# Kernel tuning notes

Measured on AMD Instinct MI355X. Metric: run time of the kernel, lower is better.

Reference implementation:

```python
import jax, jax.numpy as jnp
import numpy as np

B, S, H, W, DF, D, HID, ITERS = 8, 8, 64, 64, 64, 64, 128, 3
EPS = 1e-8


def build_grid(h, w):
    ranges = [np.linspace(-1.0, 1.0, num=h), np.linspace(-1.0, 1.0, num=w)]
    g = np.meshgrid(*ranges, sparse=False, indexing='xy')
    return jnp.asarray(np.stack(g, axis=-1), dtype=jnp.float32)  # [H, W, 2]


def ln(x, g, b):
    m = jnp.mean(x, axis=-1, keepdims=True)
    v = jnp.mean((x - m) ** 2, axis=-1, keepdims=True)
    return (x - m) * jax.lax.rsqrt(v + 1e-5) * g + b


def setup_inputs() -> dict:
    key = jax.random.key(0)
    ks = iter(jax.random.split(key, 64))
    def nrm(shape, s=0.02):
        return jax.random.normal(next(ks), shape, jnp.float32) * s
    inp = {}
    inp['inputs'] = jax.random.normal(next(ks), (B, H, W, DF), jnp.float32)
    # learned slot inits and learned per-slot position / scale factors
    inp['slots_p'] = jax.random.normal(next(ks), (1, S, D), jnp.float32)
    inp['s_pos_p'] = 2.0 * jax.random.uniform(next(ks), (1, S, 2), jnp.float32) - 1.0
    inp['s_scale_p'] = 0.1 + 0.01 * jax.random.normal(next(ks), (1, S, 2), jnp.float32)
    # soft position embedding Linear(2, D)
    inp['W_pos'] = nrm((2, D)); inp['b_pos'] = jnp.zeros((D,), jnp.float32)
    # q/k/v projections
    inp['Wq'] = nrm((D, D)); inp['bq'] = jnp.zeros((D,), jnp.float32)
    inp['Wk'] = nrm((DF, D)); inp['bk'] = jnp.zeros((D,), jnp.float32)
    inp['Wv'] = nrm((DF, D)); inp['bv'] = jnp.zeros((D,), jnp.float32)
    # layernorms
    inp['g_in'] = jnp.ones((DF,), jnp.float32); inp['b_in'] = jnp.zeros((DF,), jnp.float32)
    inp['g_slots'] = jnp.ones((D,), jnp.float32); inp['b_slots'] = jnp.zeros((D,), jnp.float32)
    inp['g_k'] = jnp.ones((D,), jnp.float32); inp['b_k'] = jnp.zeros((D,), jnp.float32)
    inp['g_v'] = jnp.ones((D,), jnp.float32); inp['b_v'] = jnp.zeros((D,), jnp.float32)
    # shared kv MLP fc1_kv / fc2_kv
    inp['W1'] = nrm((D, 2 * D)); inp['b1'] = jnp.zeros((2 * D,), jnp.float32)
    inp['W2'] = nrm((2 * D, D)); inp['b2'] = jnp.zeros((D,), jnp.float32)
    # GRUCell (torch layout transposed to [in, 3*D])
    inp['W_ih'] = nrm((D, 3 * D)); inp['b_ih'] = jnp.zeros((3 * D,), jnp.float32)
    inp['W_hh'] = nrm((D, 3 * D)); inp['b_hh'] = jnp.zeros((3 * D,), jnp.float32)
    # residual slot MLP
    inp['g_pre'] = jnp.ones((D,), jnp.float32); inp['b_pre'] = jnp.zeros((D,), jnp.float32)
    inp['Wf1'] = nrm((D, HID)); inp['bf1'] = jnp.zeros((HID,), jnp.float32)
    inp['Wf2'] = nrm((HID, D)); inp['bf2'] = jnp.zeros((D,), jnp.float32)
    return inp


def reference(inputs, slots_p, s_pos_p, s_scale_p, W_pos, b_pos, Wq, bq, Wk, bk, Wv, bv,
              g_in, b_in, g_slots, b_slots, g_k, b_k, g_v, b_v, W1, b1, W2, b2,
              W_ih, W_hh, b_ih, b_hh, g_pre, b_pre, Wf1, bf1, Wf2, bf2):
    grid = build_grid(H, W)                 # [H, W, 2]
    grid_flat = grid.reshape(-1, 2)          # [HW, 2]
    scale = D ** (-0.5)

    x = ln(inputs, g_in, b_in)
    k0 = x @ Wk + bk                         # [B, H, W, D]
    v0 = x @ Wv + bv

    slots = jnp.broadcast_to(slots_p, (B, S, D))
    s_pos = jnp.clip(jnp.broadcast_to(s_pos_p, (B, S, 2)), -1.0, 1.0)[:, :, None, None, :]
    s_scale = jnp.clip(jnp.broadcast_to(s_scale_p, (B, S, 2)), 1e-3, 2.0)[:, :, None, None, :]

    def proj_kv(base, sp, ss, g, b):
        gr = (grid[None, None] - sp) / (ss * 5.0)      # [B, S, H, W, 2]
        pe = gr @ W_pos + b_pos                        # [B, S, H, W, D]
        t = (base[:, None] + pe).reshape(B, S, H * W, D)
        t = ln(t, g, b)
        return jax.nn.relu(t @ W1 + b1) @ W2 + b2      # [B, S, HW, D]

    for i in range(ITERS + 1):
        slots_prev = slots
        q = ln(slots, g_slots, b_slots) @ Wq + bq       # [B, S, D]
        kk = proj_kv(k0, s_pos, s_scale, g_k, b_k)
        vv = proj_kv(v0, s_pos, s_scale, g_v, b_v)
        dots = jnp.einsum('bid,bijd->bij', q, kk) * scale
        attn_mask = jax.nn.softmax(dots, axis=1) + EPS  # softmax over slot axis
        attn = attn_mask / jnp.sum(attn_mask, axis=-1, keepdims=True)
        updates = jnp.einsum('bijd,bij->bid', vv, attn)
        if i < ITERS:
            xg = updates.reshape(-1, D) @ W_ih + b_ih
            hg = slots_prev.reshape(-1, D) @ W_hh + b_hh
            ir, iz, inn = jnp.split(xg, 3, axis=-1)
            hr, hz, hn = jnp.split(hg, 3, axis=-1)
            r = jax.nn.sigmoid(ir + hr)
            z = jax.nn.sigmoid(iz + hz)
            n = jnp.tanh(inn + r * hn)
            slots = ((1.0 - z) * n + z * slots_prev.reshape(-1, D)).reshape(B, S, D)
            slots = slots + (jax.nn.relu(ln(slots, g_pre, b_pre) @ Wf1 + bf1) @ Wf2 + bf2)
        else:
            slots = slots_prev
        # update per-slot position / scale from the attention mask
        sp = jnp.einsum('bij,jd->bid', attn_mask, grid_flat) / jnp.sum(attn_mask, axis=-1, keepdims=True)
        diff = grid_flat[None, None] - sp[:, :, None]   # [B, S, HW, 2]
        am = attn_mask + 1e-8
        ss = jnp.sqrt(jnp.einsum('bij,bijd->bid', am, diff ** 2) / jnp.sum(am, axis=-1, keepdims=True))
        s_pos = sp[:, :, None, None, :]
        s_scale = jnp.clip(ss, 1e-3, 2.0)[:, :, None, None, :]
    return slots, s_pos, s_scale, attn_mask
```

## Files before the change

kernel.cpp:

```cpp
#include <hip/hip_runtime.h>
#include <math.h>

typedef __bf16 bf16_t;
typedef __bf16 bfrag __attribute__((ext_vector_type(8)));
typedef float ffrag __attribute__((ext_vector_type(4)));

__device__ __forceinline__ float wave_sum(float v) {
#pragma unroll
  for (int m = 32; m >= 1; m >>= 1) v += __shfl_xor(v, m, 64);
  return v;
}
__device__ __forceinline__ float lin_(int i) { return -1.f + (2.f * (float)i) / 63.f; }
__device__ __forceinline__ float bflo(unsigned u) { return __uint_as_float(u << 16); }
__device__ __forceinline__ float bfhi(unsigned u) { return __uint_as_float(u & 0xFFFF0000u); }

__global__ __launch_bounds__(256) void k_setup(
    const float* __restrict__ slots_p, const float* __restrict__ s_pos_p,
    const float* __restrict__ s_scale_p, const float* __restrict__ W1,
    const float* __restrict__ b1, const float* __restrict__ g_k,
    const float* __restrict__ b_k, const float* __restrict__ g_v,
    const float* __restrict__ b_v, const float* __restrict__ W_pos,
    const float* __restrict__ b_pos, const float* __restrict__ Wk,
    const float* __restrict__ Wv,
    float* __restrict__ slotsS, float* __restrict__ sposS,
    float* __restrict__ sscaleS, float* __restrict__ momentsHsum,
    bf16_t* __restrict__ W1kT, bf16_t* __restrict__ W1vT,
    bf16_t* __restrict__ WkT, bf16_t* __restrict__ WvT,
    float4* __restrict__ nckA, float* __restrict__ nckB,
    float4* __restrict__ ncvA, float* __restrict__ ncvB,
    float* __restrict__ possum) {
  int t = threadIdx.x;
  for (int i = t; i < 8512; i += 256) momentsHsum[i] = 0.f;
  for (int i = t; i < 4096; i += 256) slotsS[i] = slots_p[i & 511];
  if (t < 128) {
    sposS[t] = fminf(fmaxf(s_pos_p[t & 15], -1.f), 1.f);
    sscaleS[t] = fminf(fmaxf(s_scale_p[t & 15], 0.001f), 2.f);
  }
  for (int i = t; i < 4096; i += 256) {
    int n = i >> 6, d = i & 63;
    WkT[i] = (bf16_t)Wk[d * 64 + n];
    WvT[i] = (bf16_t)Wv[d * 64 + n];
  }
  if (t < 128) {
    int n = t;
    float wxk = 0, wyk = 0, wbk = 0, uk = 0, sk = 0;
    float wxv = 0, wyv = 0, wbv = 0, uv = 0, sv = 0;
    for (int c = 0; c < 64; ++c) {
      float w = W1[c * 128 + n];
      float wk = g_k[c] * w, wv = g_v[c] * w;
      W1kT[n * 64 + c] = (bf16_t)wk;
      W1vT[n * 64 + c] = (bf16_t)wv;
      float px = W_pos[c], py = W_pos[64 + c], bp = b_pos[c];
      wxk += px * wk; wyk += py * wk; wbk += bp * wk; sk += wk; uk += b_k[c] * w;
      wxv += px * wv; wyv += py * wv; wbv += bp * wv; sv += wv; uv += b_v[c] * w;
    }
    nckA[n] = make_float4(wxk, wyk, wbk, uk + b1[n]); nckB[n] = sk;
    ncvA[n] = make_float4(wxv, wyv, wbv, uv + b1[n]); ncvB[n] = sv;
  }
  if (t < 64) {
    float px = W_pos[t], py = W_pos[64 + t], bp = b_pos[t];
    float s[9] = {px, py, bp, px * px, py * py, bp * bp, px * py, px * bp, py * bp};
#pragma unroll
    for (int i = 0; i < 9; ++i) {
      float v = wave_sum(s[i]);
      if (t == 0) possum[i] = v;
    }
  }
}

__device__ __forceinline__ void pass_type(
    const bf16_t xs[][72], bf16_t t0s[][72],
    const bf16_t WTl[][72], const bf16_t W1l[][72],
    const float* __restrict__ bias, const float* wpxs, const float* wpys,
    const float* bpvs, float* __restrict__ statsG, bf16_t* __restrict__ P0G,
    int j0, int wv, int lq, int ln15) {
  ffrag C[4] = {{0,0,0,0},{0,0,0,0},{0,0,0,0},{0,0,0,0}};
#pragma unroll
  for (int ks = 0; ks < 2; ++ks) {
    bfrag a = *(const bfrag*)&xs[wv * 16 + ln15][ks * 32 + lq * 8];
#pragma unroll
    for (int nt = 0; nt < 4; ++nt) {
      bfrag bb = *(const bfrag*)&WTl[nt * 16 + ln15][ks * 32 + lq * 8];
      C[nt] = __builtin_amdgcn_mfma_f32_16x16x32_bf16(a, bb, C[nt], 0, 0, 0);
    }
  }
  float kv[4][4];
  float st[5][4];
#pragma unroll
  for (int i = 0; i < 5; ++i)
#pragma unroll
    for (int rg = 0; rg < 4; ++rg) st[i][rg] = 0.f;
#pragma unroll
  for (int nt = 0; nt < 4; ++nt) {
    int n = nt * 16 + ln15;
    float bn = bias[n], pxw = wpxs[n], pyw = wpys[n], bpw = bpvs[n];
#pragma unroll
    for (int rg = 0; rg < 4; ++rg) {
      float v = C[nt][rg] + bn;
      kv[nt][rg] = v;
      st[0][rg] += v; st[1][rg] += v * v; st[2][rg] += v * pxw;
      st[3][rg] += v * pyw; st[4][rg] += v * bpw;
    }
  }
#pragma unroll
  for (int i = 0; i < 5; ++i)
#pragma unroll
    for (int rg = 0; rg < 4; ++rg) {
      float v = st[i][rg];
      v += __shfl_xor(v, 1, 64); v += __shfl_xor(v, 2, 64);
      v += __shfl_xor(v, 4, 64); v += __shfl_xor(v, 8, 64);
      st[i][rg] = v;
    }
  if (ln15 == 0) {
#pragma unroll
    for (int rg = 0; rg < 4; ++rg) {
      int j = j0 + wv * 16 + lq * 4 + rg;
#pragma unroll
      for (int i = 0; i < 5; ++i) statsG[j * 5 + i] = st[i][rg];
    }
  }
#pragma unroll
  for (int nt = 0; nt < 4; ++nt)
#pragma unroll
    for (int rg = 0; rg < 4; ++rg)
      t0s[wv * 16 + lq * 4 + rg][nt * 16 + ln15] = (bf16_t)kv[nt][rg];
  ffrag D[8] = {{0,0,0,0},{0,0,0,0},{0,0,0,0},{0,0,0,0},
                {0,0,0,0},{0,0,0,0},{0,0,0,0},{0,0,0,0}};
#pragma unroll
  for (int ks = 0; ks < 2; ++ks) {
    bfrag a = *(const bfrag*)&t0s[wv * 16 + ln15][ks * 32 + lq * 8];
#pragma unroll
    for (int nt = 0; nt < 8; ++nt) {
      bfrag bb = *(const bfrag*)&W1l[nt * 16 + ln15][ks * 32 + lq * 8];
      D[nt] = __builtin_amdgcn_mfma_f32_16x16x32_bf16(a, bb, D[nt], 0, 0, 0);
    }
  }
#pragma unroll
  for (int nt = 0; nt < 8; ++nt)
#pragma unroll
    for (int rg = 0; rg < 4; ++rg)
      P0G[(size_t)(j0 + wv * 16 + lq * 4 + rg) * 128 + nt * 16 + ln15] =
          (bf16_t)D[nt][rg];
}

__global__ __launch_bounds__(256) void k_pre(
    const float* __restrict__ inp, const float* __restrict__ g_in,
    const float* __restrict__ b_in, const float* __restrict__ bk,
    const float* __restrict__ bv, const bf16_t* __restrict__ WkT,
    const bf16_t* __restrict__ WvT, const bf16_t* __restrict__ W1kT,
    const bf16_t* __restrict__ W1vT, const float* __restrict__ W_pos,
    const float* __restrict__ b_pos,
    bf16_t* __restrict__ P0k, bf16_t* __restrict__ P0v,
    float* __restrict__ statsK, float* __restrict__ statsV,
    const float* __restrict__ slotsS, const float* __restrict__ g_slots,
    const float* __restrict__ b_slots, const float* __restrict__ Wq,
    const float* __restrict__ bq, const float* __restrict__ W2,
    const float* __restrict__ b2, float* __restrict__ w2qg,
    float* __restrict__ b2qg) {
  __shared__ bf16_t xs[64][72];
  __shared__ bf16_t t0s[64][72];
  __shared__ bf16_t WkTl[64][72];
  __shared__ bf16_t WvTl[64][72];
  __shared__ bf16_t W1kl[128][72];
  __shared__ bf16_t W1vl[128][72];
  __shared__ float wpxs[64], wpys[64], bpvs[64];
  const int tid = threadIdx.x;
  const int j0 = blockIdx.x * 64;
  for (int i = tid; i < 512; i += 256) {
    int row = i >> 3, seg = i & 7;
    *(uint4*)&WkTl[row][seg * 8] = ((const uint4*)WkT)[i];
    *(uint4*)&WvTl[row][seg * 8] = ((const uint4*)WvT)[i];
  }
  for (int i = tid; i < 1024; i += 256) {
    int row = i >> 3, seg = i & 7;
    *(uint4*)&W1kl[row][seg * 8] = ((const uint4*)W1kT)[i];
    *(uint4*)&W1vl[row][seg * 8] = ((const uint4*)W1vT)[i];
  }
  if (tid < 64) { wpxs[tid] = W_pos[tid]; wpys[tid] = W_pos[64 + tid]; bpvs[tid] = b_pos[tid]; }
  {
    const int px = tid >> 2, cg = tid & 3;
    const float* rowp = inp + (size_t)(j0 + px) * 64 + cg * 16;
    float v[16];
    *(float4*)&v[0]  = ((const float4*)rowp)[0];
    *(float4*)&v[4]  = ((const float4*)rowp)[1];
    *(float4*)&v[8]  = ((const float4*)rowp)[2];
    *(float4*)&v[12] = ((const float4*)rowp)[3];
    float s = 0.f, s2 = 0.f;
#pragma unroll
    for (int i = 0; i < 16; ++i) { s += v[i]; s2 += v[i] * v[i]; }
    s += __shfl_xor(s, 1, 64); s += __shfl_xor(s, 2, 64);
    s2 += __shfl_xor(s2, 1, 64); s2 += __shfl_xor(s2, 2, 64);
    float m = s * 0.015625f;
    float r = rsqrtf(s2 * 0.015625f - m * m + 1e-5f);
    float g[16], bb[16];
    *(float4*)&g[0]  = ((const float4*)(g_in + cg * 16))[0];
    *(float4*)&g[4]  = ((const float4*)(g_in + cg * 16))[1];
    *(float4*)&g[8]  = ((const float4*)(g_in + cg * 16))[2];
    *(float4*)&g[12] = ((const float4*)(g_in + cg * 16))[3];
    *(float4*)&bb[0]  = ((const float4*)(b_in + cg * 16))[0];
    *(float4*)&bb[4]  = ((const float4*)(b_in + cg * 16))[1];
    *(float4*)&bb[8]  = ((const float4*)(b_in + cg * 16))[2];
    *(float4*)&bb[12] = ((const float4*)(b_in + cg * 16))[3];
#pragma unroll
    for (int e = 0; e < 8; ++e) {
      float x0 = (v[2 * e] - m) * r * g[2 * e] + bb[2 * e];
      float x1 = (v[2 * e + 1] - m) * r * g[2 * e + 1] + bb[2 * e + 1];
      union { unsigned u; bf16_t h[2]; } cv;
      cv.h[0] = (bf16_t)x0; cv.h[1] = (bf16_t)x1;
      *(unsigned*)&xs[px][cg * 16 + 2 * e] = cv.u;
    }
  }
  __syncthreads();
  const int wv = tid >> 6, lane = tid & 63, lq = lane >> 4, ln15 = lane & 15;
  pass_type(xs, t0s, WkTl, W1kl, bk, wpxs, wpys, bpvs, statsK, P0k, j0, wv, lq, ln15);
  pass_type(xs, t0s, WvTl, W1vl, bv, wpxs, wpys, bpvs, statsV, P0v, j0, wv, lq, ln15);
  if (blockIdx.x < 64 && tid < 64) {
    int bs = blockIdx.x, d = tid;
    float v = slotsS[bs * 64 + d];
    float m = wave_sum(v) * 0.015625f;
    float c = v - m;
    float var = wave_sum(c * c) * 0.015625f;
    float xn = c * rsqrtf(var + 1e-5f) * g_slots[d] + b_slots[d];
    float q = bq[d];
    for (int cc = 0; cc < 64; ++cc) q = fmaf(__shfl(xn, cc, 64), Wq[cc * 64 + d], q);
    float w0 = 0.f, w1 = 0.f;
    for (int cc = 0; cc < 64; ++cc) {
      float qc = __shfl(q, cc, 64);
      w0 = fmaf(W2[d * 64 + cc], qc, w0);
      w1 = fmaf(W2[(64 + d) * 64 + cc], qc, w1);
    }
    w2qg[bs * 128 + d] = w0;
    w2qg[bs * 128 + 64 + d] = w1;
    float p = wave_sum(b2[d] * q);
    if (d == 0) b2qg[bs] = p;
  }
}

template <int LAST>
__global__ __launch_bounds__(256) void k_iter(
    const bf16_t* __restrict__ P0kg, const bf16_t* __restrict__ P0vg,
    const float* __restrict__ statsK, const float* __restrict__ statsV,
    const float4* __restrict__ nckA, const float* __restrict__ nckB,
    const float4* __restrict__ ncvA, const float* __restrict__ ncvB,
    const float* __restrict__ possum, const float* __restrict__ w2qg,
    const float* __restrict__ b2qg, const float* __restrict__ sposS,
    const float* __restrict__ sscaleS, float* __restrict__ moments,
    float* __restrict__ Hsum, float* __restrict__ outAttn) {
  __shared__ unsigned P0kl[64 * 65];
  __shared__ unsigned P0vl[64 * 65];
  __shared__ float4 nckAl[128];
  __shared__ float nckBl[128];
  __shared__ float w2qTl[128][8];
  __shared__ float4 scalV[64][9];
  __shared__ float attnS[64][10];
  __shared__ float HsumW[4][8][128];
  __shared__ float momAcc[8][5];
  const int tid = threadIdx.x;
  const int tile = blockIdx.x, b = blockIdx.y;
  const int jg0 = b * 4096 + tile * 64;
#pragma unroll
  for (int r = 0; r < 4; ++r) {
    int idx = tid + 256 * r;
    int row = idx >> 4, seg = idx & 15;
    uint4 v = ((const uint4*)P0kg)[(size_t)(jg0 + row) * 16 + seg];
    unsigned* dst = &P0kl[row * 65 + seg * 4];
    dst[0] = v.x; dst[1] = v.y; dst[2] = v.z; dst[3] = v.w;
    if (!LAST) {
      uint4 w = ((const uint4*)P0vg)[(size_t)(jg0 + row) * 16 + seg];
      unsigned* d2 = &P0vl[row * 65 + seg * 4];
      d2[0] = w.x; d2[1] = w.y; d2[2] = w.z; d2[3] = w.w;
    }
  }
  if (tid < 128) { nckAl[tid] = nckA[tid]; nckBl[tid] = nckB[tid]; }
#pragma unroll
  for (int r = 0; r < 4; ++r) {
    int idx = tid + 256 * r;
    int s = idx >> 7, n = idx & 127;
    w2qTl[n][s] = w2qg[(b * 8 + s) * 128 + n];
  }
  if (tid < 40) momAcc[tid / 5][tid % 5] = 0.f;
  float4 ncv0 = {0, 0, 0, 0}, ncv1 = {0, 0, 0, 0};
  float wsv0 = 0.f, wsv1 = 0.f;
  if (!LAST) {
    int l = tid & 63;
    ncv0 = ncvA[l]; ncv1 = ncvA[l + 64];
    wsv0 = ncvB[l]; wsv1 = ncvB[l + 64];
  }
  __syncthreads();

  const int px = tid >> 2, sp = tid & 3;
  const int jimg = tile * 64 + px;
  const float gx = lin_(jimg & 63), gy = lin_(jimg >> 6);
  const float Swx = possum[0], Swy = possum[1], Sbp = possum[2];
  const float Swx2 = possum[3], Swy2 = possum[4], Sbp2 = possum[5];
  const float Swxy = possum[6], Swxb = possum[7], Swyb = possum[8];
  float skA[5], svA[5];
#pragma unroll
  for (int i = 0; i < 5; ++i) {
    skA[i] = statsK[(size_t)(jg0 + px) * 5 + i];
    svA[i] = statsV[(size_t)(jg0 + px) * 5 + i];
  }
  float c1a[8], c2a[8], rKa[8], mrKa[8];
#pragma unroll
  for (int s = 0; s < 8; ++s) {
    int bs = b * 8 + s;
    float spx = sposS[bs * 2], spy = sposS[bs * 2 + 1];
    float rxx = 1.f / (sscaleS[bs * 2] * 5.f);
    float ryy = 1.f / (sscaleS[bs * 2 + 1] * 5.f);
    float c1 = (gx - spx) * rxx, c2 = (gy - spy) * ryy;
    float quad = c1 * c1 * Swx2 + c2 * c2 * Swy2 + Sbp2 +
                 2.f * (c1 * c2 * Swxy + c1 * Swxb + c2 * Swyb);
    float mK = (skA[0] + c1 * Swx + c2 * Swy + Sbp) * 0.015625f;
    float e2K = (skA[1] + 2.f * (c1 * skA[2] + c2 * skA[3] + skA[4]) + quad) * 0.015625f;
    float rK = rsqrtf(e2K - mK * mK + 1e-5f);
    c1a[s] = c1; c2a[s] = c2; rKa[s] = rK; mrKa[s] = mK * rK;
    if (!LAST && (s >> 1) == sp) {
      float mV = (svA[0] + c1 * Swx + c2 * Swy + Sbp) * 0.015625f;
      float e2V = (svA[1] + 2.f * (c1 * svA[2] + c2 * svA[3] + svA[4]) + quad) * 0.015625f;
      float rV = rsqrtf(e2V - mV * mV + 1e-5f);
      scalV[px][s] = make_float4(c1, c2, rV, mV * rV);
    }
  }
  float d8[8] = {0, 0, 0, 0, 0, 0, 0, 0};
#pragma unroll 4
  for (int i = 0; i < 16; ++i) {
    int k = sp * 16 + i;
    unsigned u = P0kl[px * 65 + k];
    float p0 = bflo(u), p1 = bfhi(u);
    float4 A0 = nckAl[2 * k], A1 = nckAl[2 * k + 1];
    float ws0 = nckBl[2 * k], ws1 = nckBl[2 * k + 1];
    float4 q0a = *(const float4*)&w2qTl[2 * k][0];
    float4 q0b = *(const float4*)&w2qTl[2 * k][4];
    float4 q1a = *(const float4*)&w2qTl[2 * k + 1][0];
    float4 q1b = *(const float4*)&w2qTl[2 * k + 1][4];
    float qq0[8] = {q0a.x, q0a.y, q0a.z, q0a.w, q0b.x, q0b.y, q0b.z, q0b.w};
    float qq1[8] = {q1a.x, q1a.y, q1a.z, q1a.w, q1b.x, q1b.y, q1b.z, q1b.w};
    float bm0 = p0 + A0.z, bm1 = p1 + A1.z;
#pragma unroll
    for (int s = 0; s < 8; ++s) {
      float z0 = bm0 + c1a[s] * A0.x + c2a[s] * A0.y;
      float h0 = fmaxf(fmaf(rKa[s], z0, fmaf(-mrKa[s], ws0, A0.w)), 0.f);
      d8[s] = fmaf(h0, qq0[s], d8[s]);
      float z1 = bm1 + c1a[s] * A1.x + c2a[s] * A1.y;
      float h1 = fmaxf(fmaf(rKa[s], z1, fmaf(-mrKa[s], ws1, A1.w)), 0.f);
      d8[s] = fmaf(h1, qq1[s], d8[s]);
    }
  }
#pragma unroll
  for (int s = 0; s < 8; ++s) {
    float v = d8[s];
    v += __shfl_xor(v, 1, 64);
    v += __shfl_xor(v, 2, 64);
    d8[s] = (v + b2qg[b * 8 + s]) * 0.125f;
  }
  float mx = d8[0];
#pragma unroll
  for (int s = 1; s < 8; ++s) mx = fmaxf(mx, d8[s]);
  float tt = 0.f;
  float e8[8];
#pragma unroll
  for (int s = 0; s < 8; ++s) { e8[s] = expf(d8[s] - mx); tt += e8[s]; }
  float inv = 1.f / tt;
#pragma unroll
  for (int s = 0; s < 8; ++s) e8[s] = e8[s] * inv + 1e-8f;
  float wa, wb;
  if (sp == 0) { wa = e8[0]; wb = e8[1]; }
  else if (sp == 1) { wa = e8[2]; wb = e8[3]; }
  else if (sp == 2) { wa = e8[4]; wb = e8[5]; }
  else { wa = e8[6]; wb = e8[7]; }
  *(float2*)&attnS[px][sp * 2] = make_float2(wa, wb);
  if (LAST) {
    outAttn[(size_t)(b * 8 + sp * 2) * 4096 + jimg] = wa;
    outAttn[(size_t)(b * 8 + sp * 2 + 1) * 4096 + jimg] = wb;
  }
  {
    float mm[10] = {wa, wa * gx, wa * gy, wa * gx * gx, wa * gy * gy,
                    wb, wb * gx, wb * gy, wb * gx * gx, wb * gy * gy};
#pragma unroll
    for (int i = 0; i < 10; ++i) {
      float v = mm[i];
      v += __shfl_xor(v, 4, 64); v += __shfl_xor(v, 8, 64);
      v += __shfl_xor(v, 16, 64); v += __shfl_xor(v, 32, 64);
      mm[i] = v;
    }
    if ((tid & 63) < 4) {
#pragma unroll
      for (int i = 0; i < 5; ++i) {
        atomicAdd(&momAcc[sp * 2][i], mm[i]);
        atomicAdd(&momAcc[sp * 2 + 1][i], mm[5 + i]);
      }
    }
  }
  __syncthreads();

  if (!LAST) {
    const int w = tid >> 6, l = tid & 63;
    float hacc[8][2];
#pragma unroll
    for (int s = 0; s < 8; ++s) { hacc[s][0] = 0.f; hacc[s][1] = 0.f; }
    const unsigned short* P16 = (const unsigned short*)P0vl;
#pragma unroll 2
    for (int i = 0; i < 16; ++i) {
      int j = w * 16 + i;
      float pv0 = __uint_as_float((unsigned)P16[j * 130 + l] << 16);
      float pv1 = __uint_as_float((unsigned)P16[j * 130 + 64 + l] << 16);
      float bm0 = pv0 + ncv0.z, bm1 = pv1 + ncv1.z;
#pragma unroll
      for (int s = 0; s < 8; ++s) {
        float4 sc = scalV[j][s];
        float aw = attnS[j][s];
        float z0 = bm0 + sc.x * ncv0.x + sc.y * ncv0.y;
        float h0 = fmaxf(fmaf(sc.z, z0, fmaf(-sc.w, wsv0, ncv0.w)), 0.f);
        hacc[s][0] = fmaf(aw, h0, hacc[s][0]);
        float z1 = bm1 + sc.x * ncv1.x + sc.y * ncv1.y;
        float h1 = fmaxf(fmaf(sc.z, z1, fmaf(-sc.w, wsv1, ncv1.w)), 0.f);
        hacc[s][1] = fmaf(aw, h1, hacc[s][1]);
      }
    }
#pragma unroll
    for (int s = 0; s < 8; ++s) {
      HsumW[w][s][l] = hacc[s][0];
      HsumW[w][s][l + 64] = hacc[s][1];
    }
    __syncthreads();
#pragma unroll
    for (int r = 0; r < 4; ++r) {
      int i = tid + 256 * r;
      int s = i >> 7, n = i & 127;
      float v = HsumW[0][s][n] + HsumW[1][s][n] + HsumW[2][s][n] + HsumW[3][s][n];
      atomicAdd(&Hsum[(b * 8 + s) * 128 + n], v);
    }
  }
  if (tid < 40)
    atomicAdd(&moments[(b * 8 + tid / 5) * 5 + tid % 5], momAcc[tid / 5][tid % 5]);
}

__global__ __launch_bounds__(192) void k_fin(
    float* __restrict__ moments, float* __restrict__ Hsum,
    const float* __restrict__ W2, const float* __restrict__ b2,
    const float* __restrict__ W_ih, const float* __restrict__ b_ih,
    const float* __restrict__ W_hh, const float* __restrict__ b_hh,
    const float* __restrict__ g_pre, const float* __restrict__ b_pre,
    const float* __restrict__ Wf1, const float* __restrict__ bf1,
    const float* __restrict__ Wf2, const float* __restrict__ bf2,
    const float* __restrict__ g_slots, const float* __restrict__ b_slots,
    const float* __restrict__ Wq, const float* __restrict__ bq,
    float* __restrict__ slotsS, float* __restrict__ sposS, float* __restrict__ sscaleS,
    float* __restrict__ w2qg, float* __restrict__ b2qg,
    float* __restrict__ outSlots, float* __restrict__ outSpos,
    float* __restrict__ outSscale, int last) {
  const int bs = blockIdx.x;
  const int t = threadIdx.x;
  __shared__ float hsum_s[128], upd[64], sprev[64], xg[192], hg[192];
  __shared__ float snew[64], xpre[64], hf[128], sfin[64], xn[64], qsh[64];
  const float M0 = moments[bs * 5 + 0];
  const float M1x = moments[bs * 5 + 1], M1y = moments[bs * 5 + 2];
  const float M2x = moments[bs * 5 + 3], M2y = moments[bs * 5 + 4];
  const float invM0 = 1.f / M0;
  const float spx = M1x * invM0, spy = M1y * invM0;
  const float M0a = M0 + 4096.f * 1e-8f;
  const float G2 = 1408.6772487f * 1e-8f;
  const float vx = (M2x + G2 - 2.f * spx * M1x + spx * spx * M0a) / M0a;
  const float vy = (M2y + G2 - 2.f * spy * M1y + spy * spy * M0a) / M0a;
  float ssx = sqrtf(fmaxf(vx, 0.f)), ssy = sqrtf(fmaxf(vy, 0.f));
  ssx = fminf(fmaxf(ssx, 0.001f), 2.f);
  ssy = fminf(fmaxf(ssy, 0.001f), 2.f);
  if (t == 0) {
    sposS[bs * 2 + 0] = spx; sposS[bs * 2 + 1] = spy;
    sscaleS[bs * 2 + 0] = ssx; sscaleS[bs * 2 + 1] = ssy;
    if (last) {
      outSpos[bs * 2 + 0] = spx; outSpos[bs * 2 + 1] = spy;
      outSscale[bs * 2 + 0] = ssx; outSscale[bs * 2 + 1] = ssy;
    }
  }
  if (last) {
    if (t < 64) outSlots[bs * 64 + t] = slotsS[bs * 64 + t];
    return;
  }
  if (t < 128) hsum_s[t] = Hsum[bs * 128 + t];
  if (t < 64) sprev[t] = slotsS[bs * 64 + t];
  __syncthreads();
  if (t < 128) Hsum[bs * 128 + t] = 0.f;
  if (t < 5) moments[bs * 5 + t] = 0.f;
  if (t < 64) {
    float a = 0.f;
#pragma unroll
    for (int k = 0; k < 128; ++k) a += hsum_s[k] * W2[k * 64 + t];
    upd[t] = a * invM0 + b2[t];
  }
  __syncthreads();
  {
    float a = b_ih[t], h = b_hh[t];
#pragma unroll
    for (int d = 0; d < 64; ++d) {
      a += upd[d] * W_ih[d * 192 + t];
      h += sprev[d] * W_hh[d * 192 + t];
    }
    xg[t] = a; hg[t] = h;
  }
  __syncthreads();
  if (t < 64) {
    float r = 1.f / (1.f + expf(-(xg[t] + hg[t])));
    float z = 1.f / (1.f + expf(-(xg[64 + t] + hg[64 + t])));
    float n = tanhf(xg[128 + t] + r * hg[128 + t]);
    snew[t] = (1.f - z) * n + z * sprev[t];
  }
  __syncthreads();
  if (t < 64) {
    float v = snew[t];
    float m = wave_sum(v) * 0.015625f;
    float c = v - m;
    float var = wave_sum(c * c) * 0.015625f;
    xpre[t] = c * rsqrtf(var + 1e-5f) * g_pre[t] + b_pre[t];
  }
  __syncthreads();
  if (t < 128) {
    float a = bf1[t];
#pragma unroll
    for (int d = 0; d < 64; ++d) a += xpre[d] * Wf1[d * 128 + t];
    hf[t] = fmaxf(a, 0.f);
  }
  __syncthreads();
  if (t < 64) {
    float a = bf2[t];
#pragma unroll
    for (int k = 0; k < 128; ++k) a += hf[k] * Wf2[k * 64 + t];
    float nv = snew[t] + a;
    slotsS[bs * 64 + t] = nv;
    sfin[t] = nv;
  }
  __syncthreads();
  if (t < 64) {
    float v = sfin[t];
    float m = wave_sum(v) * 0.015625f;
    float c = v - m;
    float var = wave_sum(c * c) * 0.015625f;
    xn[t] = c * rsqrtf(var + 1e-5f) * g_slots[t] + b_slots[t];
  }
  __syncthreads();
  if (t < 64) {
    float a = bq[t];
#pragma unroll
    for (int d = 0; d < 64; ++d) a += xn[d] * Wq[d * 64 + t];
    qsh[t] = a;
  }
  __syncthreads();
  if (t < 128) {
    float a = 0.f;
#pragma unroll
    for (int d = 0; d < 64; ++d) a += W2[t * 64 + d] * qsh[d];
    w2qg[bs * 128 + t] = a;
  }
  if (t < 64) {
    float p = wave_sum(b2[t] * qsh[t]);
    if (t == 0) b2qg[bs] = p;
  }
}

extern "C" void kernel_launch(void* const* d_in, const int* in_sizes, int n_in,
                              void* d_out, int out_size, void* d_ws, size_t ws_size,
                              hipStream_t stream) {
  const float* const* in = (const float* const*)d_in;
  float* ws = (float*)d_ws;
  bf16_t* P0k   = (bf16_t*)(ws + 0);
  bf16_t* P0v   = (bf16_t*)(ws + 2097152);
  float* statsK = ws + 4194304;
  float* statsV = ws + 4358144;
  float* w2qg   = ws + 4521984;
  float* b2qg   = ws + 4530176;
  float* slotsS = ws + 4530240;
  float* sposS  = ws + 4534336;
  float* sscaleS= ws + 4534464;
  float* moments= ws + 4534592;
  float* Hsum   = ws + 4534912;
  bf16_t* W1kT  = (bf16_t*)(ws + 4543104);
  bf16_t* W1vT  = (bf16_t*)(ws + 4547200);
  bf16_t* WkT   = (bf16_t*)(ws + 4551296);
  bf16_t* WvT   = (bf16_t*)(ws + 4553344);
  float4* nckA  = (float4*)(ws + 4555392);
  float* nckB   = ws + 4555904;
  float4* ncvA  = (float4*)(ws + 4556032);
  float* ncvB   = ws + 4556544;
  float* possum = ws + 4556672;

  float* out = (float*)d_out;
  float* outSlots  = out;
  float* outSpos   = out + 4096;
  float* outSscale = out + 4224;
  float* outAttn   = out + 4352;

  k_setup<<<1, 256, 0, stream>>>(in[1], in[2], in[3], in[20], in[21],
                                 in[16], in[17], in[18], in[19], in[4], in[5],
                                 in[8], in[10], slotsS, sposS, sscaleS, moments,
                                 W1kT, W1vT, WkT, WvT, nckA, nckB, ncvA, ncvB, possum);
  k_pre<<<512, 256, 0, stream>>>(in[0], in[12], in[13], in[9], in[11],
                                 WkT, WvT, W1kT, W1vT, in[4], in[5],
                                 P0k, P0v, statsK, statsV,
                                 slotsS, in[14], in[15], in[6], in[7], in[22], in[23],
                                 w2qg, b2qg);
  for (int i = 0; i < 4; ++i) {
    int last = (i == 3) ? 1 : 0;
    if (!last) {
      k_iter<0><<<dim3(64, 8), 256, 0, stream>>>(
          P0k, P0v, statsK, statsV, nckA, nckB, ncvA, ncvB, possum,
          w2qg, b2qg, sposS, sscaleS, moments, Hsum, outAttn);
    } else {
      k_iter<1><<<dim3(64, 8), 256, 0, stream>>>(
          P0k, P0v, statsK, statsV, nckA, nckB, ncvA, ncvB, possum,
          w2qg, b2qg, sposS, sscaleS, moments, Hsum, outAttn);
    }
    k_fin<<<64, 192, 0, stream>>>(moments, Hsum, in[22], in[23], in[24], in[25],
                                  in[26], in[27], in[28], in[29], in[30], in[31],
                                  in[32], in[33], in[14], in[15], in[6], in[7],
                                  slotsS, sposS, sscaleS, w2qg, b2qg,
                                  outSlots, outSpos, outSscale, last);
  }
}
```

Before: 300.4 us.

## Fold setup kernel into k_pre and replace atomics with per-tile partial buffers

```diff
diff --git a/kernel.cpp b/kernel.cpp
--- a/kernel.cpp
+++ b/kernel.cpp
@@ -13,60 +13,6 @@
 __device__ __forceinline__ float lin_(int i) { return -1.f + (2.f * (float)i) / 63.f; }
 __device__ __forceinline__ float bflo(unsigned u) { return __uint_as_float(u << 16); }
 __device__ __forceinline__ float bfhi(unsigned u) { return __uint_as_float(u & 0xFFFF0000u); }
-
-__global__ __launch_bounds__(256) void k_setup(
-    const float* __restrict__ slots_p, const float* __restrict__ s_pos_p,
-    const float* __restrict__ s_scale_p, const float* __restrict__ W1,
-    const float* __restrict__ b1, const float* __restrict__ g_k,
-    const float* __restrict__ b_k, const float* __restrict__ g_v,
-    const float* __restrict__ b_v, const float* __restrict__ W_pos,
-    const float* __restrict__ b_pos, const float* __restrict__ Wk,
-    const float* __restrict__ Wv,
-    float* __restrict__ slotsS, float* __restrict__ sposS,
-    float* __restrict__ sscaleS, float* __restrict__ momentsHsum,
-    bf16_t* __restrict__ W1kT, bf16_t* __restrict__ W1vT,
-    bf16_t* __restrict__ WkT, bf16_t* __restrict__ WvT,
-    float4* __restrict__ nckA, float* __restrict__ nckB,
-    float4* __restrict__ ncvA, float* __restrict__ ncvB,
-    float* __restrict__ possum) {
-  int t = threadIdx.x;
-  for (int i = t; i < 8512; i += 256) momentsHsum[i] = 0.f;
-  for (int i = t; i < 4096; i += 256) slotsS[i] = slots_p[i & 511];
-  if (t < 128) {
-    sposS[t] = fminf(fmaxf(s_pos_p[t & 15], -1.f), 1.f);
-    sscaleS[t] = fminf(fmaxf(s_scale_p[t & 15], 0.001f), 2.f);
-  }
-  for (int i = t; i < 4096; i += 256) {
-    int n = i >> 6, d = i & 63;
-    WkT[i] = (bf16_t)Wk[d * 64 + n];
-    WvT[i] = (bf16_t)Wv[d * 64 + n];
-  }
-  if (t < 128) {
-    int n = t;
-    float wxk = 0, wyk = 0, wbk = 0, uk = 0, sk = 0;
-    float wxv = 0, wyv = 0, wbv = 0, uv = 0, sv = 0;
-    for (int c = 0; c < 64; ++c) {
-      float w = W1[c * 128 + n];
-      float wk = g_k[c] * w, wv = g_v[c] * w;
-      W1kT[n * 64 + c] = (bf16_t)wk;
-      W1vT[n * 64 + c] = (bf16_t)wv;
-      float px = W_pos[c], py = W_pos[64 + c], bp = b_pos[c];
-      wxk += px * wk; wyk += py * wk; wbk += bp * wk; sk += wk; uk += b_k[c] * w;
-      wxv += px * wv; wyv += py * wv; wbv += bp * wv; sv += wv; uv += b_v[c] * w;
-    }
-    nckA[n] = make_float4(wxk, wyk, wbk, uk + b1[n]); nckB[n] = sk;
-    ncvA[n] = make_float4(wxv, wyv, wbv, uv + b1[n]); ncvB[n] = sv;
-  }
-  if (t < 64) {
-    float px = W_pos[t], py = W_pos[64 + t], bp = b_pos[t];
-    float s[9] = {px, py, bp, px * px, py * py, bp * bp, px * py, px * bp, py * bp};
-#pragma unroll
-    for (int i = 0; i < 9; ++i) {
-      float v = wave_sum(s[i]);
-      if (t == 0) possum[i] = v;
-    }
-  }
-}
 
 __device__ __forceinline__ void pass_type(
     const bf16_t xs[][72], bf16_t t0s[][72],
@@ -146,17 +92,24 @@
 __global__ __launch_bounds__(256) void k_pre(
     const float* __restrict__ inp, const float* __restrict__ g_in,
     const float* __restrict__ b_in, const float* __restrict__ bk,
-    const float* __restrict__ bv, const bf16_t* __restrict__ WkT,
-    const bf16_t* __restrict__ WvT, const bf16_t* __restrict__ W1kT,
-    const bf16_t* __restrict__ W1vT, const float* __restrict__ W_pos,
-    const float* __restrict__ b_pos,
+    const float* __restrict__ bv, const float* __restrict__ Wk,
+    const float* __restrict__ Wv, const float* __restrict__ W1,
+    const float* __restrict__ g_k, const float* __restrict__ g_v,
+    const float* __restrict__ W_pos, const float* __restrict__ b_pos,
     bf16_t* __restrict__ P0k, bf16_t* __restrict__ P0v,
     float* __restrict__ statsK, float* __restrict__ statsV,
-    const float* __restrict__ slotsS, const float* __restrict__ g_slots,
+    const float* __restrict__ slots_p, const float* __restrict__ g_slots,
     const float* __restrict__ b_slots, const float* __restrict__ Wq,
     const float* __restrict__ bq, const float* __restrict__ W2,
     const float* __restrict__ b2, float* __restrict__ w2qg,
-    float* __restrict__ b2qg) {
+    float* __restrict__ b2qg,
+    const float* __restrict__ b_k, const float* __restrict__ b_v,
+    const float* __restrict__ b1, const float* __restrict__ s_pos_p,
+    const float* __restrict__ s_scale_p,
+    float4* __restrict__ nckA, float* __restrict__ nckB,
+    float4* __restrict__ ncvA, float* __restrict__ ncvB,
+    float* __restrict__ possum, float* __restrict__ sposS,
+    float* __restrict__ sscaleS, float* __restrict__ slotsS) {
   __shared__ bf16_t xs[64][72];
   __shared__ bf16_t t0s[64][72];
   __shared__ bf16_t WkTl[64][72];
@@ -166,15 +119,16 @@
   __shared__ float wpxs[64], wpys[64], bpvs[64];
   const int tid = threadIdx.x;
   const int j0 = blockIdx.x * 64;
-  for (int i = tid; i < 512; i += 256) {
-    int row = i >> 3, seg = i & 7;
-    *(uint4*)&WkTl[row][seg * 8] = ((const uint4*)WkT)[i];
-    *(uint4*)&WvTl[row][seg * 8] = ((const uint4*)WvT)[i];
-  }
-  for (int i = tid; i < 1024; i += 256) {
-    int row = i >> 3, seg = i & 7;
-    *(uint4*)&W1kl[row][seg * 8] = ((const uint4*)W1kT)[i];
-    *(uint4*)&W1vl[row][seg * 8] = ((const uint4*)W1vT)[i];
+  for (int i = tid; i < 4096; i += 256) {
+    int n = i & 63, d = i >> 6;
+    WkTl[n][d] = (bf16_t)Wk[i];
+    WvTl[n][d] = (bf16_t)Wv[i];
+  }
+  for (int i = tid; i < 8192; i += 256) {
+    int n = i & 127, c = i >> 7;
+    float w = W1[i];
+    W1kl[n][c] = (bf16_t)(g_k[c] * w);
+    W1vl[n][c] = (bf16_t)(g_v[c] * w);
   }
   if (tid < 64) { wpxs[tid] = W_pos[tid]; wpys[tid] = W_pos[64 + tid]; bpvs[tid] = b_pos[tid]; }
   {
@@ -213,10 +167,11 @@
   __syncthreads();
   const int wv = tid >> 6, lane = tid & 63, lq = lane >> 4, ln15 = lane & 15;
   pass_type(xs, t0s, WkTl, W1kl, bk, wpxs, wpys, bpvs, statsK, P0k, j0, wv, lq, ln15);
+  __syncthreads();
   pass_type(xs, t0s, WvTl, W1vl, bv, wpxs, wpys, bpvs, statsV, P0v, j0, wv, lq, ln15);
   if (blockIdx.x < 64 && tid < 64) {
     int bs = blockIdx.x, d = tid;
-    float v = slotsS[bs * 64 + d];
+    float v = slots_p[(bs & 7) * 64 + d];
     float m = wave_sum(v) * 0.015625f;
     float c = v - m;
     float var = wave_sum(c * c) * 0.015625f;
@@ -234,6 +189,44 @@
     float p = wave_sum(b2[d] * q);
     if (d == 0) b2qg[bs] = p;
   }
+  if (blockIdx.x == 508 && tid < 128) {
+    int n = tid;
+    float wx = 0, wy = 0, wb = 0, u = 0, sk = 0;
+    for (int c = 0; c < 64; ++c) {
+      float w = W1[c * 128 + n];
+      float wf = g_k[c] * w;
+      float px = W_pos[c], py = W_pos[64 + c], bp = b_pos[c];
+      wx += px * wf; wy += py * wf; wb += bp * wf; sk += wf; u += b_k[c] * w;
+    }
+    nckA[n] = make_float4(wx, wy, wb, u + b1[n]); nckB[n] = sk;
+  }
+  if (blockIdx.x == 509 && tid < 128) {
+    int n = tid;
+    float wx = 0, wy = 0, wb = 0, u = 0, sv = 0;
+    for (int c = 0; c < 64; ++c) {
+      float w = W1[c * 128 + n];
+      float wf = g_v[c] * w;
+      float px = W_pos[c], py = W_pos[64 + c], bp = b_pos[c];
+      wx += px * wf; wy += py * wf; wb += bp * wf; sv += wf; u += b_v[c] * w;
+    }
+    ncvA[n] = make_float4(wx, wy, wb, u + b1[n]); ncvB[n] = sv;
+  }
+  if (blockIdx.x == 510) {
+    if (tid < 64) {
+      float px = W_pos[tid], py = W_pos[64 + tid], bp = b_pos[tid];
+      float s9[9] = {px, py, bp, px * px, py * py, bp * bp, px * py, px * bp, py * bp};
+#pragma unroll
+      for (int i = 0; i < 9; ++i) {
+        float v = wave_sum(s9[i]);
+        if (tid == 0) possum[i] = v;
+      }
+    }
+    if (tid < 128) {
+      sposS[tid] = fminf(fmaxf(s_pos_p[tid & 15], -1.f), 1.f);
+      sscaleS[tid] = fminf(fmaxf(s_scale_p[tid & 15], 0.001f), 2.f);
+    }
+    for (int i = tid; i < 4096; i += 256) slotsS[i] = slots_p[i & 511];
+  }
 }
 
 template <int LAST>
@@ -244,8 +237,8 @@
     const float4* __restrict__ ncvA, const float* __restrict__ ncvB,
     const float* __restrict__ possum, const float* __restrict__ w2qg,
     const float* __restrict__ b2qg, const float* __restrict__ sposS,
-    const float* __restrict__ sscaleS, float* __restrict__ moments,
-    float* __restrict__ Hsum, float* __restrict__ outAttn) {
+    const float* __restrict__ sscaleS, float* __restrict__ momP,
+    float* __restrict__ HsumP, float* __restrict__ outAttn) {
   __shared__ unsigned P0kl[64 * 65];
   __shared__ unsigned P0vl[64 * 65];
   __shared__ float4 nckAl[128];
@@ -428,15 +421,16 @@
       int i = tid + 256 * r;
       int s = i >> 7, n = i & 127;
       float v = HsumW[0][s][n] + HsumW[1][s][n] + HsumW[2][s][n] + HsumW[3][s][n];
-      atomicAdd(&Hsum[(b * 8 + s) * 128 + n], v);
+      HsumP[((size_t)(b * 8 + s) * 64 + tile) * 128 + n] = v;
     }
   }
   if (tid < 40)
-    atomicAdd(&moments[(b * 8 + tid / 5) * 5 + tid % 5], momAcc[tid / 5][tid % 5]);
+    momP[((size_t)(b * 8 + tid / 5) * 64 + tile) * 5 + tid % 5] =
+        momAcc[tid / 5][tid % 5];
 }
 
 __global__ __launch_bounds__(192) void k_fin(
-    float* __restrict__ moments, float* __restrict__ Hsum,
+    const float* __restrict__ momP, const float* __restrict__ HsumP,
     const float* __restrict__ W2, const float* __restrict__ b2,
     const float* __restrict__ W_ih, const float* __restrict__ b_ih,
     const float* __restrict__ W_hh, const float* __restrict__ b_hh,
@@ -453,9 +447,27 @@
   const int t = threadIdx.x;
   __shared__ float hsum_s[128], upd[64], sprev[64], xg[192], hg[192];
   __shared__ float snew[64], xpre[64], hf[128], sfin[64], xn[64], qsh[64];
-  const float M0 = moments[bs * 5 + 0];
-  const float M1x = moments[bs * 5 + 1], M1y = moments[bs * 5 + 2];
-  const float M2x = moments[bs * 5 + 3], M2y = moments[bs * 5 + 4];
+  __shared__ float mom_s[5];
+  if (t < 64) {
+    const float* mp = momP + ((size_t)bs * 64 + t) * 5;
+    float m0 = mp[0], m1 = mp[1], m2 = mp[2], m3 = mp[3], m4 = mp[4];
+    m0 = wave_sum(m0); m1 = wave_sum(m1); m2 = wave_sum(m2);
+    m3 = wave_sum(m3); m4 = wave_sum(m4);
+    if (t == 0) { mom_s[0] = m0; mom_s[1] = m1; mom_s[2] = m2; mom_s[3] = m3; mom_s[4] = m4; }
+    if (!last) sprev[t] = slotsS[bs * 64 + t];
+  }
+  if (!last && t >= 64) {
+    int n = t - 64;
+    const float* hp = HsumP + (size_t)bs * 8192 + n;
+    float a = 0.f;
+#pragma unroll 8
+    for (int tile = 0; tile < 64; ++tile) a += hp[tile * 128];
+    hsum_s[n] = a;
+  }
+  __syncthreads();
+  const float M0 = mom_s[0];
+  const float M1x = mom_s[1], M1y = mom_s[2];
+  const float M2x = mom_s[3], M2y = mom_s[4];
   const float invM0 = 1.f / M0;
   const float spx = M1x * invM0, spy = M1y * invM0;
   const float M0a = M0 + 4096.f * 1e-8f;
@@ -477,11 +489,6 @@
     if (t < 64) outSlots[bs * 64 + t] = slotsS[bs * 64 + t];
     return;
   }
-  if (t < 128) hsum_s[t] = Hsum[bs * 128 + t];
-  if (t < 64) sprev[t] = slotsS[bs * 64 + t];
-  __syncthreads();
-  if (t < 128) Hsum[bs * 128 + t] = 0.f;
-  if (t < 5) moments[bs * 5 + t] = 0.f;
   if (t < 64) {
     float a = 0.f;
 #pragma unroll
@@ -560,6 +567,7 @@
 extern "C" void kernel_launch(void* const* d_in, const int* in_sizes, int n_in,
                               void* d_out, int out_size, void* d_ws, size_t ws_size,
                               hipStream_t stream) {
+  (void)in_sizes; (void)n_in; (void)out_size; (void)ws_size;
   const float* const* in = (const float* const*)d_in;
   float* ws = (float*)d_ws;
   bf16_t* P0k   = (bf16_t*)(ws + 0);
@@ -571,17 +579,13 @@
   float* slotsS = ws + 4530240;
   float* sposS  = ws + 4534336;
   float* sscaleS= ws + 4534464;
-  float* moments= ws + 4534592;
-  float* Hsum   = ws + 4534912;
-  bf16_t* W1kT  = (bf16_t*)(ws + 4543104);
-  bf16_t* W1vT  = (bf16_t*)(ws + 4547200);
-  bf16_t* WkT   = (bf16_t*)(ws + 4551296);
-  bf16_t* WvT   = (bf16_t*)(ws + 4553344);
   float4* nckA  = (float4*)(ws + 4555392);
   float* nckB   = ws + 4555904;
   float4* ncvA  = (float4*)(ws + 4556032);
   float* ncvB   = ws + 4556544;
   float* possum = ws + 4556672;
+  float* HsumP  = ws + 4560896;
+  float* momP   = ws + 5085184;
 
   float* out = (float*)d_out;
   float* outSlots  = out;
@@ -589,27 +593,24 @@
   float* outSscale = out + 4224;
   float* outAttn   = out + 4352;
 
-  k_setup<<<1, 256, 0, stream>>>(in[1], in[2], in[3], in[20], in[21],
-                                 in[16], in[17], in[18], in[19], in[4], in[5],
-                                 in[8], in[10], slotsS, sposS, sscaleS, moments,
-                                 W1kT, W1vT, WkT, WvT, nckA, nckB, ncvA, ncvB, possum);
-  k_pre<<<512, 256, 0, stream>>>(in[0], in[12], in[13], in[9], in[11],
-                                 WkT, WvT, W1kT, W1vT, in[4], in[5],
-                                 P0k, P0v, statsK, statsV,
-                                 slotsS, in[14], in[15], in[6], in[7], in[22], in[23],
-                                 w2qg, b2qg);
+  k_pre<<<512, 256, 0, stream>>>(
+      in[0], in[12], in[13], in[9], in[11], in[8], in[10], in[20], in[16], in[18],
+      in[4], in[5], P0k, P0v, statsK, statsV,
+      in[1], in[14], in[15], in[6], in[7], in[22], in[23], w2qg, b2qg,
+      in[17], in[19], in[21], in[2], in[3],
+      nckA, nckB, ncvA, ncvB, possum, sposS, sscaleS, slotsS);
   for (int i = 0; i < 4; ++i) {
     int last = (i == 3) ? 1 : 0;
     if (!last) {
       k_iter<0><<<dim3(64, 8), 256, 0, stream>>>(
           P0k, P0v, statsK, statsV, nckA, nckB, ncvA, ncvB, possum,
-          w2qg, b2qg, sposS, sscaleS, moments, Hsum, outAttn);
+          w2qg, b2qg, sposS, sscaleS, momP, HsumP, outAttn);
     } else {
       k_iter<1><<<dim3(64, 8), 256, 0, stream>>>(
           P0k, P0v, statsK, statsV, nckA, nckB, ncvA, ncvB, possum,
-          w2qg, b2qg, sposS, sscaleS, moments, Hsum, outAttn);
-    }
-    k_fin<<<64, 192, 0, stream>>>(moments, Hsum, in[22], in[23], in[24], in[25],
+          w2qg, b2qg, sposS, sscaleS, momP, HsumP, outAttn);
+    }
+    k_fin<<<64, 192, 0, stream>>>(momP, HsumP, in[22], in[23], in[24], in[25],
                                   in[26], in[27], in[28], in[29], in[30], in[31],
                                   in[32], in[33], in[14], in[15], in[6], in[7],
                                   slotsS, sposS, sscaleS, w2qg, b2qg,
```

Result: faster. 287.1 us (-4.4%).
